# Kernel optimization log

Hardware: AMD Instinct MI355X
Metric: run time of the kernel (lower is better)

## Reference

```python
import jax, jax.numpy as jnp
import numpy as np

D_MODEL = 1024
NUM_HEADS = 16
HEAD = D_MODEL // NUM_HEADS
SCALE = float(np.sqrt(D_MODEL))  # note: sqrt(d_model), as in source
LN_EPS = 1e-5


def setup_inputs() -> dict:
    key = jax.random.key(0)
    ks = jax.random.split(key, 12)
    B, Sq, Skv = 2, 2048, 2048
    s = 0.02
    return {
        "x": jax.random.normal(ks[0], (B, Sq, D_MODEL), jnp.float32),
        "enc_output": jax.random.normal(ks[1], (B, Skv, D_MODEL), jnp.float32),
        "Wq": jax.random.normal(ks[2], (D_MODEL, D_MODEL), jnp.float32) * s,
        "bq": jnp.zeros((D_MODEL,), jnp.float32),
        "Wk": jax.random.normal(ks[3], (D_MODEL, D_MODEL), jnp.float32) * s,
        "bk": jnp.zeros((D_MODEL,), jnp.float32),
        "Wv": jax.random.normal(ks[4], (D_MODEL, D_MODEL), jnp.float32) * s,
        "bv": jnp.zeros((D_MODEL,), jnp.float32),
        "Wo": jax.random.normal(ks[5], (D_MODEL, D_MODEL), jnp.float32) * s,
        "bo": jnp.zeros((D_MODEL,), jnp.float32),
        "gamma": jnp.ones((D_MODEL,), jnp.float32),
        "beta": jnp.zeros((D_MODEL,), jnp.float32),
    }


def _split_heads(t):
    B, S, _ = t.shape
    return t.reshape(B, S, NUM_HEADS, HEAD).transpose(0, 2, 1, 3)  # [B,H,S,hd]


def reference(x, enc_output, Wq, bq, Wk, bk, Wv, bv, Wo, bo, gamma, beta):
    q = _split_heads(x @ Wq.T + bq)           # [B,H,Sq,hd]
    k = _split_heads(enc_output @ Wk.T + bk)  # [B,H,Skv,hd]
    v = _split_heads(enc_output @ Wv.T + bv)  # [B,H,Skv,hd]
    scores = jnp.einsum("bhqd,bhkd->bhqk", q, k) / SCALE
    attn_weights = jax.nn.softmax(scores, axis=-1)  # dropout p=0 -> identity
    ctx = jnp.einsum("bhqk,bhkd->bhqd", attn_weights, v)
    B, H, Sq, hd = ctx.shape
    ctx = ctx.transpose(0, 2, 1, 3).reshape(B, Sq, H * hd)
    proj = ctx @ Wo.T + bo
    y = x + proj
    mu = jnp.mean(y, axis=-1, keepdims=True)
    var = jnp.var(y, axis=-1, keepdims=True)
    out = (y - mu) * jax.lax.rsqrt(var + LN_EPS) * gamma + beta
    return out, attn_weights
```

## Files before the change

### kernel.cpp

```cpp
#include <hip/hip_runtime.h>

typedef __attribute__((ext_vector_type(4))) float f32x4;
typedef __attribute__((ext_vector_type(8))) short bf16x8;
typedef __attribute__((ext_vector_type(4))) short s16x4;
typedef unsigned short u16;

#define GLOAD_LDS16(g, l)                                                      \
  __builtin_amdgcn_global_load_lds(                                            \
      (__attribute__((address_space(1))) const void*)(g),                      \
      (__attribute__((address_space(3))) void*)(l), 16, 0, 0)

static __device__ __forceinline__ u16 f2b(float f) {
  unsigned u = __builtin_bit_cast(unsigned, f);
  unsigned r = (u + 0x7fffu + ((u >> 16) & 1u)) >> 16;
  return (u16)r;
}

static __device__ __forceinline__ f32x4 mfma16(bf16x8 a, bf16x8 b, f32x4 c) {
  return __builtin_amdgcn_mfma_f32_16x16x32_bf16(a, b, c, 0, 0, 0);
}

static __device__ __forceinline__ int fsw(int row) {
  return (row & 7) ^ ((row & 8) >> 1);
}

__global__ __launch_bounds__(256) void cvt_bf16(const float* __restrict__ in,
                                                u16* __restrict__ out, int n4) {
  int i = blockIdx.x * 256 + threadIdx.x;
  int stride = gridDim.x * 256;
  for (; i < n4; i += stride) {
    float4 v = ((const float4*)in)[i];
    s16x4 o;
    o[0] = (short)f2b(v.x);
    o[1] = (short)f2b(v.y);
    o[2] = (short)f2b(v.z);
    o[3] = (short)f2b(v.w);
    ((s16x4*)out)[i] = o;
  }
}

#define QSCALE 0.0450842200278f
__global__ __launch_bounds__(256) void gemm_qkv3(
    const u16* __restrict__ xb, const u16* __restrict__ eb,
    const u16* __restrict__ Wqb, const u16* __restrict__ Wkb,
    const u16* __restrict__ Wvb, const float* __restrict__ bq,
    const float* __restrict__ bk, const float* __restrict__ bv,
    u16* __restrict__ Qd, u16* __restrict__ Kd, u16* __restrict__ Vtd) {
  __shared__ __align__(16) u16 As[128 * 32];
  __shared__ __align__(16) u16 Bs[128 * 32];
  const int K = 1024;
  int z = blockIdx.z;
  const u16* A = (z == 0) ? xb : eb;
  const u16* W = (z == 0) ? Wqb : (z == 1) ? Wkb : Wvb;
  const float* bias = (z == 0) ? bq : (z == 1) ? bk : bv;

  int tid = threadIdx.x;
  int w = tid >> 6, lane = tid & 63;
  int wr = w >> 1, wc = w & 1;
  int r16 = lane & 15, c4 = lane >> 4;
  int m0 = blockIdx.y * 128, n0 = blockIdx.x * 128;
  int srow = tid >> 2;
  int scol = (tid & 3) * 8;

  f32x4 acc[4][4] = {};

  const u16* ga0 = A + (size_t)(m0 + srow) * K + scol;
  const u16* gb0 = W + (size_t)(n0 + srow) * K + scol;
  char* asb = (char*)As + w * 1024;
  char* bsb = (char*)Bs + w * 1024;

  for (int k0 = 0; k0 < K; k0 += 32) {
    GLOAD_LDS16(ga0 + k0, asb);
    GLOAD_LDS16(ga0 + 64 * K + k0, asb + 4096);
    GLOAD_LDS16(gb0 + k0, bsb);
    GLOAD_LDS16(gb0 + 64 * K + k0, bsb + 4096);
    __syncthreads();
    bf16x8 af[4], bfr[4];
#pragma unroll
    for (int i = 0; i < 4; ++i)
      af[i] = *(const bf16x8*)(As + (wr * 64 + i * 16 + r16) * 32 + c4 * 8);
#pragma unroll
    for (int j = 0; j < 4; ++j)
      bfr[j] = *(const bf16x8*)(Bs + (wc * 64 + j * 16 + r16) * 32 + c4 * 8);
#pragma unroll
    for (int i = 0; i < 4; ++i)
#pragma unroll
      for (int j = 0; j < 4; ++j) acc[i][j] = mfma16(af[i], bfr[j], acc[i][j]);
    __syncthreads();
  }

  if (z < 2) {
    float oscale = (z == 0) ? QSCALE : 1.0f;
    u16* dst = (z == 0) ? Qd : Kd;
#pragma unroll
    for (int i = 0; i < 4; ++i) {
      int m = m0 + wr * 64 + i * 16 + c4 * 4;
      int b = m >> 11, s = m & 2047;
#pragma unroll
      for (int j = 0; j < 4; ++j) {
        int n = n0 + wc * 64 + j * 16 + r16;
        int h = n >> 6, d = n & 63;
        float bv = bias[n];
        u16* dp = dst + (((size_t)(b * 16 + h) * 2048 + s) * 64 + d);
#pragma unroll
        for (int r = 0; r < 4; ++r)
          dp[(size_t)r * 64] = f2b((acc[i][j][r] + bv) * oscale);
      }
    }
  } else {
#pragma unroll
    for (int i = 0; i < 4; ++i) {
      int m = m0 + wr * 64 + i * 16 + c4 * 4;
      int b = m >> 11, s = m & 2047;
#pragma unroll
      for (int j = 0; j < 4; ++j) {
        int n = n0 + wc * 64 + j * 16 + r16;
        int h = n >> 6, d = n & 63;
        float bv = bias[n];
        s16x4 o4;
#pragma unroll
        for (int r = 0; r < 4; ++r) o4[r] = (short)f2b(acc[i][j][r] + bv);
        *(s16x4*)(Vtd + ((size_t)((b * 16 + h) * 64 + d)) * 2048 + s) = o4;
      }
    }
  }
}

__global__ __launch_bounds__(256) void gemm_out(const u16* __restrict__ A,
                                                const u16* __restrict__ W,
                                                const float* __restrict__ bias,
                                                const float* __restrict__ X,
                                                float* __restrict__ Y) {
  __shared__ __align__(16) u16 As[128 * 32];
  __shared__ __align__(16) u16 Bs[128 * 32];
  const int K = 1024;
  int tid = threadIdx.x;
  int w = tid >> 6, lane = tid & 63;
  int wr = w >> 1, wc = w & 1;
  int r16 = lane & 15, c4 = lane >> 4;
  int m0 = blockIdx.y * 128, n0 = blockIdx.x * 128;
  int srow = tid >> 2;
  int scol = (tid & 3) * 8;

  f32x4 acc[4][4] = {};

  const u16* ga0 = A + (size_t)(m0 + srow) * K + scol;
  const u16* gb0 = W + (size_t)(n0 + srow) * K + scol;
  char* asb = (char*)As + w * 1024;
  char* bsb = (char*)Bs + w * 1024;

  for (int k0 = 0; k0 < K; k0 += 32) {
    GLOAD_LDS16(ga0 + k0, asb);
    GLOAD_LDS16(ga0 + 64 * K + k0, asb + 4096);
    GLOAD_LDS16(gb0 + k0, bsb);
    GLOAD_LDS16(gb0 + 64 * K + k0, bsb + 4096);
    __syncthreads();
    bf16x8 af[4], bfr[4];
#pragma unroll
    for (int i = 0; i < 4; ++i)
      af[i] = *(const bf16x8*)(As + (wr * 64 + i * 16 + r16) * 32 + c4 * 8);
#pragma unroll
    for (int j = 0; j < 4; ++j)
      bfr[j] = *(const bf16x8*)(Bs + (wc * 64 + j * 16 + r16) * 32 + c4 * 8);
#pragma unroll
    for (int i = 0; i < 4; ++i)
#pragma unroll
      for (int j = 0; j < 4; ++j) acc[i][j] = mfma16(af[i], bfr[j], acc[i][j]);
    __syncthreads();
  }

#pragma unroll
  for (int i = 0; i < 4; ++i) {
    int m = m0 + wr * 64 + i * 16 + c4 * 4;
#pragma unroll
    for (int j = 0; j < 4; ++j) {
      int n = n0 + wc * 64 + j * 16 + r16;
      float bv = bias[n];
#pragma unroll
      for (int r = 0; r < 4; ++r) {
        size_t idx = (size_t)(m + r) * 1024 + n;
        Y[idx] = acc[i][j][r] + bv + X[idx];
      }
    }
  }
}

__global__ __launch_bounds__(256, 2) void attn_k(const u16* __restrict__ Q,
                                                 const u16* __restrict__ Kg,
                                                 const u16* __restrict__ Vt,
                                                 float* __restrict__ attnw,
                                                 u16* __restrict__ ctx) {
  __shared__ __align__(16) u16 Klds[2][64 * 64];
  __shared__ __align__(16) u16 Vlds[2][64 * 64];

  int tid = threadIdx.x;
  int w = tid >> 6, lane = tid & 63;
  int r16 = lane & 15, c4 = lane >> 4;
  int id = blockIdx.x;
  int bh = id & 31, qt = id >> 5;
  int b = bh >> 4, h = bh & 15;
  int q0 = qt * 128 + w * 32;

  const u16* Qp = Q + ((size_t)bh * 2048 + q0) * 64;
  const u16* Kp = Kg + (size_t)bh * 2048 * 64;
  const u16* Vp = Vt + (size_t)bh * 64 * 2048;

  bf16x8 qf[2][2];
#pragma unroll
  for (int hh = 0; hh < 2; ++hh)
#pragma unroll
    for (int ch = 0; ch < 2; ++ch)
      qf[hh][ch] = *(const bf16x8*)(Qp + (size_t)(hh * 16 + r16) * 64 +
                                    ch * 32 + c4 * 8);

  int perm0 = ((r16 >> 2) << 3) + (r16 & 3);
  int srow0 = w * 8 + (lane >> 3);
  int sc = lane & 7;

#define STAGE_K(bufi, kv)                                                      \
  {                                                                            \
    _Pragma("unroll") for (int i = 0; i < 2; ++i) {                            \
      int row = i * 32 + srow0;                                                \
      int ch = sc ^ fsw(row);                                                  \
      GLOAD_LDS16(Kp + (size_t)((kv) + row) * 64 + ch * 8,                     \
                  (u16*)&Klds[bufi][0] + w * 512 + i * 2048);                  \
    }                                                                          \
  }
#define STAGE_V(bufi, kv)                                                      \
  {                                                                            \
    _Pragma("unroll") for (int i = 0; i < 2; ++i) {                            \
      int row = i * 32 + srow0;                                                \
      int ch = sc ^ fsw(row);                                                  \
      GLOAD_LDS16(Vp + (size_t)row * 2048 + (kv) + ch * 8,                     \
                  (u16*)&Vlds[bufi][0] + w * 512 + i * 2048);                  \
    }                                                                          \
  }
#define LDSF(base, row, chunk)                                                 \
  (*(const bf16x8*)((base) + (row) * 64 + (((chunk) ^ fsw(row)) << 3)))

  float sumA = 0.f, sumB = 0.f;
  STAGE_K(0, 0);
  __syncthreads();
  int buf = 0;
  for (int kv0 = 0; kv0 < 2048; kv0 += 64) {
    if (kv0 + 64 < 2048) STAGE_K(buf ^ 1, kv0 + 64);
    const u16* Kb = &Klds[buf][0];
#pragma unroll
    for (int s = 0; s < 2; ++s) {
      int ra = s * 32 + perm0;
      bf16x8 k00 = LDSF(Kb, ra, c4);
      bf16x8 k01 = LDSF(Kb, ra, c4 + 4);
      bf16x8 k10 = LDSF(Kb, ra + 4, c4);
      bf16x8 k11 = LDSF(Kb, ra + 4, c4 + 4);
      f32x4 s0A = {}, s1A = {}, s0B = {}, s1B = {};
      __builtin_amdgcn_s_setprio(1);
      s0A = mfma16(k00, qf[0][0], s0A);
      s0A = mfma16(k01, qf[0][1], s0A);
      s1A = mfma16(k10, qf[0][0], s1A);
      s1A = mfma16(k11, qf[0][1], s1A);
      s0B = mfma16(k00, qf[1][0], s0B);
      s0B = mfma16(k01, qf[1][1], s0B);
      s1B = mfma16(k10, qf[1][0], s1B);
      s1B = mfma16(k11, qf[1][1], s1B);
      __builtin_amdgcn_s_setprio(0);
#pragma unroll
      for (int r = 0; r < 4; ++r) {
        sumA += __builtin_amdgcn_exp2f(s0A[r]) + __builtin_amdgcn_exp2f(s1A[r]);
        sumB += __builtin_amdgcn_exp2f(s0B[r]) + __builtin_amdgcn_exp2f(s1B[r]);
      }
    }
    __syncthreads();
    buf ^= 1;
  }
  sumA += __shfl_xor(sumA, 16, 64);
  sumA += __shfl_xor(sumA, 32, 64);
  sumB += __shfl_xor(sumB, 16, 64);
  sumB += __shfl_xor(sumB, 32, 64);
  float nlsA = -__log2f(sumA);
  float nlsB = -__log2f(sumB);

  f32x4 oA[4] = {}, oB[4] = {};
  float* apA = attnw + ((size_t)bh * 2048 + q0 + r16) * 2048;
  float* apB = apA + (size_t)16 * 2048;
  STAGE_K(0, 0);
  STAGE_V(0, 0);
  __syncthreads();
  buf = 0;
  for (int kv0 = 0; kv0 < 2048; kv0 += 64) {
    if (kv0 + 64 < 2048) {
      STAGE_K(buf ^ 1, kv0 + 64);
      STAGE_V(buf ^ 1, kv0 + 64);
    }
    const u16* Kb = &Klds[buf][0];
    const u16* Vb = &Vlds[buf][0];
#pragma unroll
    for (int s = 0; s < 2; ++s) {
      int ra = s * 32 + perm0;
      bf16x8 k00 = LDSF(Kb, ra, c4);
      bf16x8 k01 = LDSF(Kb, ra, c4 + 4);
      bf16x8 k10 = LDSF(Kb, ra + 4, c4);
      bf16x8 k11 = LDSF(Kb, ra + 4, c4 + 4);
      f32x4 s0A = {}, s1A = {}, s0B = {}, s1B = {};
      __builtin_amdgcn_s_setprio(1);
      s0A = mfma16(k00, qf[0][0], s0A);
      s0A = mfma16(k01, qf[0][1], s0A);
      s1A = mfma16(k10, qf[0][0], s1A);
      s1A = mfma16(k11, qf[0][1], s1A);
      s0B = mfma16(k00, qf[1][0], s0B);
      s0B = mfma16(k01, qf[1][1], s0B);
      s1B = mfma16(k10, qf[1][0], s1B);
      s1B = mfma16(k11, qf[1][1], s1B);
      __builtin_amdgcn_s_setprio(0);
      f32x4 p0A, p1A, p0B, p1B;
#pragma unroll
      for (int r = 0; r < 4; ++r) {
        p0A[r] = __builtin_amdgcn_exp2f(s0A[r] + nlsA);
        p1A[r] = __builtin_amdgcn_exp2f(s1A[r] + nlsA);
        p0B[r] = __builtin_amdgcn_exp2f(s0B[r] + nlsB);
        p1B[r] = __builtin_amdgcn_exp2f(s1B[r] + nlsB);
      }
      int kvc = kv0 + s * 32 + c4 * 8;
      *(f32x4*)(apA + kvc) = p0A;
      *(f32x4*)(apA + kvc + 4) = p1A;
      *(f32x4*)(apB + kvc) = p0B;
      *(f32x4*)(apB + kvc + 4) = p1B;
      bf16x8 pfA, pfB;
#pragma unroll
      for (int r = 0; r < 4; ++r) {
        pfA[r] = (short)f2b(p0A[r]);
        pfA[r + 4] = (short)f2b(p1A[r]);
        pfB[r] = (short)f2b(p0B[r]);
        pfB[r + 4] = (short)f2b(p1B[r]);
      }
      bf16x8 v0 = LDSF(Vb, 0 * 16 + r16, s * 4 + c4);
      bf16x8 v1 = LDSF(Vb, 1 * 16 + r16, s * 4 + c4);
      bf16x8 v2 = LDSF(Vb, 2 * 16 + r16, s * 4 + c4);
      bf16x8 v3 = LDSF(Vb, 3 * 16 + r16, s * 4 + c4);
      __builtin_amdgcn_s_setprio(1);
      oA[0] = mfma16(pfA, v0, oA[0]);
      oA[1] = mfma16(pfA, v1, oA[1]);
      oA[2] = mfma16(pfA, v2, oA[2]);
      oA[3] = mfma16(pfA, v3, oA[3]);
      oB[0] = mfma16(pfB, v0, oB[0]);
      oB[1] = mfma16(pfB, v1, oB[1]);
      oB[2] = mfma16(pfB, v2, oB[2]);
      oB[3] = mfma16(pfB, v3, oB[3]);
      __builtin_amdgcn_s_setprio(0);
    }
    __syncthreads();
    buf ^= 1;
  }

#pragma unroll
  for (int dt = 0; dt < 4; ++dt)
#pragma unroll
    for (int r = 0; r < 4; ++r) {
      ctx[((size_t)(b * 2048 + q0 + c4 * 4 + r)) * 1024 + h * 64 + dt * 16 +
          r16] = f2b(oA[dt][r]);
      ctx[((size_t)(b * 2048 + q0 + 16 + c4 * 4 + r)) * 1024 + h * 64 +
          dt * 16 + r16] = f2b(oB[dt][r]);
    }
#undef STAGE_K
#undef STAGE_V
#undef LDSF
}

__global__ __launch_bounds__(256) void ln_k(const float* __restrict__ Y,
                                            const float* __restrict__ gamma,
                                            const float* __restrict__ beta,
                                            float* __restrict__ out) {
  int row = blockIdx.x * 4 + (threadIdx.x >> 6);
  int lane = threadIdx.x & 63;
  const float* yr = Y + (size_t)row * 1024;
  float4 v[4];
  float sum = 0.f, sq = 0.f;
#pragma unroll
  for (int i = 0; i < 4; ++i) {
    v[i] = *(const float4*)(yr + i * 256 + lane * 4);
    sum += v[i].x + v[i].y + v[i].z + v[i].w;
    sq += v[i].x * v[i].x + v[i].y * v[i].y + v[i].z * v[i].z + v[i].w * v[i].w;
  }
#pragma unroll
  for (int m = 1; m < 64; m <<= 1) {
    sum += __shfl_xor(sum, m, 64);
    sq += __shfl_xor(sq, m, 64);
  }
  float mu = sum * (1.f / 1024.f);
  float var = sq * (1.f / 1024.f) - mu * mu;
  float rs = rsqrtf(var + 1e-5f);
  float* orow = out + (size_t)row * 1024;
#pragma unroll
  for (int i = 0; i < 4; ++i) {
    int c = i * 256 + lane * 4;
    float4 g = *(const float4*)(gamma + c);
    float4 be = *(const float4*)(beta + c);
    float4 o;
    o.x = (v[i].x - mu) * rs * g.x + be.x;
    o.y = (v[i].y - mu) * rs * g.y + be.y;
    o.z = (v[i].z - mu) * rs * g.z + be.z;
    o.w = (v[i].w - mu) * rs * g.w + be.w;
    *(float4*)(orow + c) = o;
  }
}

extern "C" void kernel_launch(void* const* d_in, const int* in_sizes, int n_in,
                              void* d_out, int out_size, void* d_ws,
                              size_t ws_size, hipStream_t stream) {
  const float* x = (const float*)d_in[0];
  const float* enc = (const float*)d_in[1];
  const float* Wq = (const float*)d_in[2];
  const float* bq = (const float*)d_in[3];
  const float* Wk = (const float*)d_in[4];
  const float* bk = (const float*)d_in[5];
  const float* Wv = (const float*)d_in[6];
  const float* bv = (const float*)d_in[7];
  const float* Wo = (const float*)d_in[8];
  const float* bo = (const float*)d_in[9];
  const float* gamma = (const float*)d_in[10];
  const float* beta = (const float*)d_in[11];

  float* out = (float*)d_out;
  float* attnw = out + (size_t)4194304;

  char* ws = (char*)d_ws;
  u16* xb = (u16*)(ws + (size_t)0);
  u16* eb = (u16*)(ws + ((size_t)8 << 20));
  u16* Wqb = (u16*)(ws + ((size_t)16 << 20));
  u16* Wkb = (u16*)(ws + ((size_t)18 << 20));
  u16* Wvb = (u16*)(ws + ((size_t)20 << 20));
  u16* Wob = (u16*)(ws + ((size_t)22 << 20));
  u16* Qws = (u16*)(ws + ((size_t)24 << 20));
  u16* Kws = (u16*)(ws + ((size_t)32 << 20));
  u16* Vt = (u16*)(ws + ((size_t)48 << 20));
  u16* ctx = (u16*)(ws + ((size_t)40 << 20));
  float* Yws = (float*)(ws + (size_t)0);

  cvt_bf16<<<dim3(1024), 256, 0, stream>>>(x, xb, 1048576);
  cvt_bf16<<<dim3(1024), 256, 0, stream>>>(enc, eb, 1048576);
  cvt_bf16<<<dim3(256), 256, 0, stream>>>(Wq, Wqb, 262144);
  cvt_bf16<<<dim3(256), 256, 0, stream>>>(Wk, Wkb, 262144);
  cvt_bf16<<<dim3(256), 256, 0, stream>>>(Wv, Wvb, 262144);
  cvt_bf16<<<dim3(256), 256, 0, stream>>>(Wo, Wob, 262144);

  gemm_qkv3<<<dim3(8, 32, 3), 256, 0, stream>>>(xb, eb, Wqb, Wkb, Wvb, bq, bk,
                                                bv, Qws, Kws, Vt);

  attn_k<<<dim3(512), 256, 0, stream>>>(Qws, Kws, Vt, attnw, ctx);

  gemm_out<<<dim3(8, 32), 256, 0, stream>>>(ctx, Wob, bo, x, Yws);

  ln_k<<<dim3(1024), 256, 0, stream>>>(Yws, gamma, beta, out);
}
```

Measured before the change: 310.8 us.

## Merge weight conversions, pack bf16 converts, and relax attention barrier waits

Combines the four weight fp32-to-bf16 conversion launches into one 2D-grid kernel to cut launch overhead. In the attention kernel, replaces per-element software bf16 rounding with the hardware packed convert instruction. It also moves the attention-weight global stores after the PV MFMAs and replaces __syncthreads with an explicit vmcnt wait that leaves the eight stores outstanding, so the barrier no longer waits on them. The risk is that the vmcnt(8) count depends on the exact number and order of outstanding vector-memory ops. If the compiler schedules them differently, the wait can be too loose for the LDS staging loads or too strict.

```diff
diff --git a/kernel.cpp b/kernel.cpp
--- a/kernel.cpp
+++ b/kernel.cpp
@@ -3,6 +3,7 @@
 typedef __attribute__((ext_vector_type(4))) float f32x4;
 typedef __attribute__((ext_vector_type(8))) short bf16x8;
 typedef __attribute__((ext_vector_type(4))) short s16x4;
+typedef __attribute__((ext_vector_type(4))) unsigned u32x4;
 typedef unsigned short u16;
 
 #define GLOAD_LDS16(g, l)                                                      \
@@ -16,6 +17,12 @@
   return (u16)r;
 }
 
+static __device__ __forceinline__ unsigned pk2(float lo, float hi) {
+  unsigned r;
+  asm("v_cvt_pk_bf16_f32 %0, %1, %2" : "=v"(r) : "v"(lo), "v"(hi));
+  return r;
+}
+
 static __device__ __forceinline__ f32x4 mfma16(bf16x8 a, bf16x8 b, f32x4 c) {
   return __builtin_amdgcn_mfma_f32_16x16x32_bf16(a, b, c, 0, 0, 0);
 }
@@ -26,6 +33,31 @@
 
 __global__ __launch_bounds__(256) void cvt_bf16(const float* __restrict__ in,
                                                 u16* __restrict__ out, int n4) {
+  int i = blockIdx.x * 256 + threadIdx.x;
+  int stride = gridDim.x * 256;
+  for (; i < n4; i += stride) {
+    float4 v = ((const float4*)in)[i];
+    s16x4 o;
+    o[0] = (short)f2b(v.x);
+    o[1] = (short)f2b(v.y);
+    o[2] = (short)f2b(v.z);
+    o[3] = (short)f2b(v.w);
+    ((s16x4*)out)[i] = o;
+  }
+}
+
+__global__ __launch_bounds__(256) void cvt_w4(const float* __restrict__ w0,
+                                              const float* __restrict__ w1,
+                                              const float* __restrict__ w2,
+                                              const float* __restrict__ w3,
+                                              u16* __restrict__ o0,
+                                              u16* __restrict__ o1,
+                                              u16* __restrict__ o2,
+                                              u16* __restrict__ o3) {
+  int y = blockIdx.y;
+  const float* in = (y == 0) ? w0 : (y == 1) ? w1 : (y == 2) ? w2 : w3;
+  u16* out = (y == 0) ? o0 : (y == 1) ? o1 : (y == 2) ? o2 : o3;
+  const int n4 = 262144;
   int i = blockIdx.x * 256 + threadIdx.x;
   int stride = gridDim.x * 256;
   for (; i < n4; i += stride) {
@@ -237,10 +269,15 @@
   }
 #define LDSF(base, row, chunk)                                                 \
   (*(const bf16x8*)((base) + (row) * 64 + (((chunk) ^ fsw(row)) << 3)))
+#define WAIT_BAR(n)                                                            \
+  {                                                                            \
+    asm volatile("s_waitcnt vmcnt(" #n ")" ::: "memory");                      \
+    __builtin_amdgcn_s_barrier();                                              \
+  }
 
   float sumA = 0.f, sumB = 0.f;
   STAGE_K(0, 0);
-  __syncthreads();
+  WAIT_BAR(0);
   int buf = 0;
   for (int kv0 = 0; kv0 < 2048; kv0 += 64) {
     if (kv0 + 64 < 2048) STAGE_K(buf ^ 1, kv0 + 64);
@@ -269,7 +306,7 @@
         sumB += __builtin_amdgcn_exp2f(s0B[r]) + __builtin_amdgcn_exp2f(s1B[r]);
       }
     }
-    __syncthreads();
+    WAIT_BAR(0);
     buf ^= 1;
   }
   sumA += __shfl_xor(sumA, 16, 64);
@@ -284,7 +321,7 @@
   float* apB = apA + (size_t)16 * 2048;
   STAGE_K(0, 0);
   STAGE_V(0, 0);
-  __syncthreads();
+  WAIT_BAR(0);
   buf = 0;
   for (int kv0 = 0; kv0 < 2048; kv0 += 64) {
     if (kv0 + 64 < 2048) {
@@ -319,19 +356,17 @@
         p0B[r] = __builtin_amdgcn_exp2f(s0B[r] + nlsB);
         p1B[r] = __builtin_amdgcn_exp2f(s1B[r] + nlsB);
       }
-      int kvc = kv0 + s * 32 + c4 * 8;
-      *(f32x4*)(apA + kvc) = p0A;
-      *(f32x4*)(apA + kvc + 4) = p1A;
-      *(f32x4*)(apB + kvc) = p0B;
-      *(f32x4*)(apB + kvc + 4) = p1B;
-      bf16x8 pfA, pfB;
-#pragma unroll
-      for (int r = 0; r < 4; ++r) {
-        pfA[r] = (short)f2b(p0A[r]);
-        pfA[r + 4] = (short)f2b(p1A[r]);
-        pfB[r] = (short)f2b(p0B[r]);
-        pfB[r + 4] = (short)f2b(p1B[r]);
-      }
+      u32x4 pkA, pkB;
+      pkA[0] = pk2(p0A[0], p0A[1]);
+      pkA[1] = pk2(p0A[2], p0A[3]);
+      pkA[2] = pk2(p1A[0], p1A[1]);
+      pkA[3] = pk2(p1A[2], p1A[3]);
+      pkB[0] = pk2(p0B[0], p0B[1]);
+      pkB[1] = pk2(p0B[2], p0B[3]);
+      pkB[2] = pk2(p1B[0], p1B[1]);
+      pkB[3] = pk2(p1B[2], p1B[3]);
+      bf16x8 pfA = __builtin_bit_cast(bf16x8, pkA);
+      bf16x8 pfB = __builtin_bit_cast(bf16x8, pkB);
       bf16x8 v0 = LDSF(Vb, 0 * 16 + r16, s * 4 + c4);
       bf16x8 v1 = LDSF(Vb, 1 * 16 + r16, s * 4 + c4);
       bf16x8 v2 = LDSF(Vb, 2 * 16 + r16, s * 4 + c4);
@@ -346,8 +381,13 @@
       oB[2] = mfma16(pfB, v2, oB[2]);
       oB[3] = mfma16(pfB, v3, oB[3]);
       __builtin_amdgcn_s_setprio(0);
-    }
-    __syncthreads();
+      int kvc = kv0 + s * 32 + c4 * 8;
+      *(f32x4*)(apA + kvc) = p0A;
+      *(f32x4*)(apA + kvc + 4) = p1A;
+      *(f32x4*)(apB + kvc) = p0B;
+      *(f32x4*)(apB + kvc + 4) = p1B;
+    }
+    WAIT_BAR(8);
     buf ^= 1;
   }
 
@@ -363,6 +403,7 @@
 #undef STAGE_K
 #undef STAGE_V
 #undef LDSF
+#undef WAIT_BAR
 }
 
 __global__ __launch_bounds__(256) void ln_k(const float* __restrict__ Y,
@@ -437,10 +478,7 @@
 
   cvt_bf16<<<dim3(1024), 256, 0, stream>>>(x, xb, 1048576);
   cvt_bf16<<<dim3(1024), 256, 0, stream>>>(enc, eb, 1048576);
-  cvt_bf16<<<dim3(256), 256, 0, stream>>>(Wq, Wqb, 262144);
-  cvt_bf16<<<dim3(256), 256, 0, stream>>>(Wk, Wkb, 262144);
-  cvt_bf16<<<dim3(256), 256, 0, stream>>>(Wv, Wvb, 262144);
-  cvt_bf16<<<dim3(256), 256, 0, stream>>>(Wo, Wob, 262144);
+  cvt_w4<<<dim3(256, 4), 256, 0, stream>>>(Wq, Wk, Wv, Wo, Wqb, Wkb, Wvb, Wob);
 
   gemm_qkv3<<<dim3(8, 32, 3), 256, 0, stream>>>(xb, eb, Wqb, Wkb, Wvb, bq, bk,
                                                 bv, Qws, Kws, Vt);
```

Result: faster. 304.5 us (-2.0%).
